# Kernel tuning notes

Hardware: AMD Instinct MI355X
Metric: run time of the kernel (lower is better)

The kernel has to match this reference:

```python
import jax, jax.numpy as jnp
import numpy as np

BS = 2048; N = 16; IN = 128; H = 128; M = 64; A = 32; IMSG = 64; NNH = 256; NA = 30; CB = 64

def _lin(x, w, b):
    return x @ w.T + b

def _bn(x, g, b):
    # BatchNorm1d in training mode: batch statistics, biased variance, eps=1e-5
    m = x.mean(0)
    v = x.var(0)
    return (x - m) / jnp.sqrt(v + 1e-5) * g + b

_lrelu = jax.nn.leaky_relu  # default negative_slope=0.01 matches torch LeakyReLU


def setup_inputs() -> dict:
    key = jax.random.key(0)
    ks = iter(jax.random.split(key, 32))
    def w(shape):
        return jax.random.normal(next(ks), shape, jnp.float32) / np.sqrt(shape[-1]).astype(np.float32)
    R = BS * N
    return {
        'inputs': jax.random.normal(next(ks), (R, IN), jnp.float32),
        'hidden_state': jax.random.normal(next(ks), (R, H), jnp.float32),
        'latent_state': jax.random.normal(next(ks), (R, CB), jnp.float32),
        'eps': jax.random.normal(next(ks), (R, M), jnp.float32),
        'fc1_w': w((H, IN)), 'fc1_b': jnp.zeros((H,), jnp.float32),
        'w_ih': w((3 * H, H)), 'w_hh': w((3 * H, H)),
        'b_ih': jnp.zeros((3 * H,), jnp.float32), 'b_hh': jnp.zeros((3 * H,), jnp.float32),
        'lse_w1': w((H, CB)), 'lse_b1': jnp.zeros((H,), jnp.float32),
        'lse_w2': w((H, H)), 'lse_b2': jnp.zeros((H,), jnp.float32),
        'me_w1': w((NNH, 2 * H)), 'me_b1': jnp.zeros((NNH,), jnp.float32),
        'me_g': jnp.ones((NNH,), jnp.float32), 'me_beta': jnp.zeros((NNH,), jnp.float32),
        'me_w2': w((2 * M, NNH)), 'me_b2': jnp.zeros((2 * M,), jnp.float32),
        'k_w': w((A, H)), 'k_b': jnp.zeros((A,), jnp.float32),
        'q_w': w((A, M)), 'q_b': jnp.zeros((A,), jnp.float32),
        'v_w1': w((NNH, H + M)), 'v_b1': jnp.zeros((NNH,), jnp.float32),
        'v_w2': w((IMSG, NNH)), 'v_b2': jnp.zeros((IMSG,), jnp.float32),
        'fc2_w': w((NA, 2 * H + IMSG * N)), 'fc2_b': jnp.zeros((NA,), jnp.float32),
        'n_agents': N,
    }


def reference(inputs, hidden_state, latent_state, eps,
              fc1_w, fc1_b, w_ih, w_hh, b_ih, b_hh,
              lse_w1, lse_b1, lse_w2, lse_b2,
              me_w1, me_b1, me_g, me_beta, me_w2, me_b2,
              k_w, k_b, q_w, q_b, v_w1, v_b1, v_w2, v_b2,
              fc2_w, fc2_b, n_agents):
    n = n_agents
    R = inputs.shape[0]
    bs = R // n
    # calc_hidden: fc1 + relu, then GRUCell
    x = jax.nn.relu(_lin(inputs, fc1_w, fc1_b))
    gi = _lin(x, w_ih, b_ih)
    gh = _lin(hidden_state, w_hh, b_hh)
    ir, iz, inn = jnp.split(gi, 3, axis=-1)
    hr, hz, hn = jnp.split(gh, 3, axis=-1)
    r = jax.nn.sigmoid(ir + hr)
    z = jax.nn.sigmoid(iz + hz)
    ng = jnp.tanh(inn + r * hn)
    h = ng + z * (hidden_state - ng)  # [R, H]
    # latent_state_encoder
    latent_emb = _lin(jax.nn.relu(_lin(latent_state, lse_w1, lse_b1)), lse_w2, lse_b2)
    le_d = jax.lax.stop_gradient(latent_emb)  # .detach() in source
    # msg_encoder -> clamped Normal params -> rsample
    t = _lrelu(_bn(_lin(jnp.concatenate([h, le_d], -1), me_w1, me_b1), me_g, me_beta))
    t = _lrelu(_lin(t, me_w2, me_b2))
    Md = eps.shape[-1]
    mean = jnp.clip(t[:, :Md], -1.0, 1.0)
    std = jnp.clip(t[:, Md:], 0.5, 1.0)
    pm = mean + std * eps  # personal_msg per agent, [R, M]
    # attn_message_integration: value/query at pair (i,j) depend only on sender j,
    # so compute once per sender and broadcast (same math as repeat in source).
    value = _lin(_lrelu(_lin(jnp.concatenate([h, pm], -1), v_w1, v_b1)), v_w2, v_b2).reshape(bs, n, -1)
    keyv = _lin(h, k_w, k_b).reshape(bs, n, -1)
    qv = _lin(pm, q_w, q_b).reshape(bs, n, -1)
    kh = keyv / jnp.maximum(jnp.linalg.norm(keyv, axis=-1, keepdims=True), 1e-8)
    qh = qv / jnp.maximum(jnp.linalg.norm(qv, axis=-1, keepdims=True), 1e-8)
    alpha = jax.nn.softmax(jnp.einsum('bia,bja->bij', kh, qh), axis=-1)  # cosine attn
    diag_mask = 1.0 - jnp.eye(n, dtype=alpha.dtype)  # zero self-messages
    msg = (alpha * diag_mask)[..., None] * value[:, None, :, :]  # [bs, n, n, IMSG]
    msg = msg.reshape(R, -1)
    return _lin(jnp.concatenate([h, latent_emb, msg], -1), fc2_w, fc2_b)  # q: [R, NA]
```

## Files before the change

### kernel.cpp

```cpp
#include <hip/hip_runtime.h>
#include <math.h>

namespace {
constexpr int R_ = 32768;
constexpr int N_ = 16;
constexpr int NA_ = 30;
constexpr int BSB_ = R_ / N_;
constexpr int NB64_ = R_ / 64;
}

typedef __bf16 bf16x8 __attribute__((ext_vector_type(8)));
typedef float f32x4 __attribute__((ext_vector_type(4)));

__device__ inline unsigned int f2bf(float f) {
    unsigned int u = __float_as_uint(f);
    return (u + 0x7fffu + ((u >> 16) & 1u)) >> 16;
}
__device__ inline float bf2f(unsigned int us) {
    return __uint_as_float(us << 16);
}
__device__ inline unsigned int pack2(float a, float b) {
    return f2bf(a) | (f2bf(b) << 16);
}
__device__ inline uint4 pack8(float4 f0, float4 f1) {
    uint4 u;
    u.x = pack2(f0.x, f0.y); u.y = pack2(f0.z, f0.w);
    u.z = pack2(f1.x, f1.y); u.w = pack2(f1.z, f1.w);
    return u;
}
__device__ inline float fsig(float x)  { return __builtin_amdgcn_rcpf(1.f + __expf(-x)); }
__device__ inline float ftanh(float x) { return 1.f - 2.f * __builtin_amdgcn_rcpf(__expf(2.f * x) + 1.f); }

__device__ __forceinline__ bf16x8 lda_frag(const uint4* At, int KC, int row, int c) {
    return __builtin_bit_cast(bf16x8, At[(row * KC + c) ^ (row & 7)]);
}
__device__ __forceinline__ bf16x8 ldb_frag(const unsigned short* W, int row, int rstride, int c) {
    return __builtin_bit_cast(bf16x8, *(const uint4*)(W + (size_t)row * rstride + (size_t)c * 8));
}

namespace woff {
constexpr unsigned fc1 = 0;
constexpr unsigned ih  = 16384;
constexpr unsigned hh  = 65536;
constexpr unsigned l1  = 114688;
constexpr unsigned l2  = 122880;
constexpr unsigned m1  = 139264;
constexpr unsigned m2  = 204800;
constexpr unsigned kw  = 237568;
constexpr unsigned qw  = 241664;
constexpr unsigned v1  = 243712;
constexpr unsigned v2  = 292864;
constexpr unsigned f2  = 309248;
constexpr unsigned total = 347648;
}

__global__ __launch_bounds__(256)
void wcvt_kernel(const float* __restrict__ fc1_w, const float* __restrict__ w_ih,
                 const float* __restrict__ w_hh, const float* __restrict__ lse_w1,
                 const float* __restrict__ lse_w2, const float* __restrict__ me_w1,
                 const float* __restrict__ me_w2, const float* __restrict__ k_w,
                 const float* __restrict__ q_w, const float* __restrict__ v_w1,
                 const float* __restrict__ v_w2, const float* __restrict__ fc2_w,
                 unsigned short* __restrict__ dst)
{
    unsigned i = blockIdx.x * 256 + threadIdx.x;
    if (i >= woff::total) return;
    const float* src; unsigned base;
    if      (i < woff::ih) { src = fc1_w;  base = woff::fc1; }
    else if (i < woff::hh) { src = w_ih;   base = woff::ih; }
    else if (i < woff::l1) { src = w_hh;   base = woff::hh; }
    else if (i < woff::l2) { src = lse_w1; base = woff::l1; }
    else if (i < woff::m1) { src = lse_w2; base = woff::l2; }
    else if (i < woff::m2) { src = me_w1;  base = woff::m1; }
    else if (i < woff::kw) { src = me_w2;  base = woff::m2; }
    else if (i < woff::qw) { src = k_w;    base = woff::kw; }
    else if (i < woff::v1) { src = q_w;    base = woff::qw; }
    else if (i < woff::v2) { src = v_w1;   base = woff::v1; }
    else if (i < woff::f2) { src = v_w2;   base = woff::v2; }
    else                   { src = fc2_w;  base = woff::f2; }
    dst[i] = (unsigned short)f2bf(src[i - base]);
}

__global__ __launch_bounds__(512, 4)
void stage1(const float* __restrict__ inputs, const float* __restrict__ hidden,
            const unsigned short* __restrict__ fc1w, const float* __restrict__ fc1_b,
            const unsigned short* __restrict__ wih, const unsigned short* __restrict__ whh,
            const float* __restrict__ b_ih, const float* __restrict__ b_hh,
            unsigned short* __restrict__ hb,
            const float* __restrict__ latent,
            const unsigned short* __restrict__ w1b, const float* __restrict__ b1,
            const unsigned short* __restrict__ w2b, const float* __restrict__ b2,
            unsigned short* __restrict__ leb)
{
    __shared__ uint4 shbuf[64 * 48];
    const int tid = threadIdx.x;
    const int lane = tid & 63, w = tid >> 6;
    const int m = lane & 15, g = lane >> 4;

    if (blockIdx.x < (unsigned)NB64_) {
        uint4* Ain   = shbuf;
        uint4* Atile = shbuf + 64 * 16;
        const int r0 = blockIdx.x * 64;

        for (int idx = tid; idx < 64 * 16; idx += 512) {
            int row = idx >> 4, c = idx & 15;
            const float4* p = (const float4*)(inputs + (size_t)(r0 + row) * 128 + c * 8);
            Ain[(row * 16 + c) ^ (row & 7)] = pack8(p[0], p[1]);
            const float4* ph = (const float4*)(hidden + (size_t)(r0 + row) * 128 + c * 8);
            Atile[(row * 32 + (16 + c)) ^ (row & 7)] = pack8(ph[0], ph[1]);
        }
        __syncthreads();

        {
            f32x4 acc[4] = {};
            #pragma unroll
            for (int ks = 0; ks < 4; ++ks) {
                bf16x8 bf = ldb_frag(fc1w, w * 16 + m, 128, ks * 4 + g);
                #pragma unroll
                for (int fr = 0; fr < 4; ++fr) {
                    bf16x8 af = lda_frag(Ain, 16, fr * 16 + m, ks * 4 + g);
                    acc[fr] = __builtin_amdgcn_mfma_f32_16x16x32_bf16(af, bf, acc[fr], 0, 0, 0);
                }
            }
            int col = w * 16 + m;
            float bv = fc1_b[col];
            int c = col >> 3, el = col & 7;
            #pragma unroll
            for (int fr = 0; fr < 4; ++fr) {
                #pragma unroll
                for (int i = 0; i < 4; ++i) {
                    int row = fr * 16 + g * 4 + i;
                    float v = acc[fr][i] + bv;
                    v = v > 0.f ? v : 0.f;
                    ((unsigned short*)Atile)[((row * 32 + c) ^ (row & 7)) * 8 + el] =
                        (unsigned short)f2bf(v);
                }
            }
        }
        __syncthreads();

        {
            f32x4 rr[4] = {}, zz[4] = {}, ni[4] = {}, nh[4] = {};
            const int ro = w * 16 + m;
            #pragma unroll
            for (int ks = 0; ks < 4; ++ks) {
                bf16x8 brr = ldb_frag(wih, ro, 128, ks * 4 + g);
                bf16x8 bzz = ldb_frag(wih, 128 + ro, 128, ks * 4 + g);
                bf16x8 bnn = ldb_frag(wih, 256 + ro, 128, ks * 4 + g);
                #pragma unroll
                for (int fr = 0; fr < 4; ++fr) {
                    bf16x8 af = lda_frag(Atile, 32, fr * 16 + m, ks * 4 + g);
                    rr[fr] = __builtin_amdgcn_mfma_f32_16x16x32_bf16(af, brr, rr[fr], 0, 0, 0);
                    zz[fr] = __builtin_amdgcn_mfma_f32_16x16x32_bf16(af, bzz, zz[fr], 0, 0, 0);
                    ni[fr] = __builtin_amdgcn_mfma_f32_16x16x32_bf16(af, bnn, ni[fr], 0, 0, 0);
                }
            }
            #pragma unroll
            for (int ks = 0; ks < 4; ++ks) {
                bf16x8 brr = ldb_frag(whh, ro, 128, ks * 4 + g);
                bf16x8 bzz = ldb_frag(whh, 128 + ro, 128, ks * 4 + g);
                bf16x8 bnn = ldb_frag(whh, 256 + ro, 128, ks * 4 + g);
                #pragma unroll
                for (int fr = 0; fr < 4; ++fr) {
                    bf16x8 af = lda_frag(Atile, 32, fr * 16 + m, 16 + ks * 4 + g);
                    rr[fr] = __builtin_amdgcn_mfma_f32_16x16x32_bf16(af, brr, rr[fr], 0, 0, 0);
                    zz[fr] = __builtin_amdgcn_mfma_f32_16x16x32_bf16(af, bzz, zz[fr], 0, 0, 0);
                    nh[fr] = __builtin_amdgcn_mfma_f32_16x16x32_bf16(af, bnn, nh[fr], 0, 0, 0);
                }
            }
            {
                int c = ro;
                float brz = b_ih[c] + b_hh[c];
                float bzz2 = b_ih[128 + c] + b_hh[128 + c];
                float bin = b_ih[256 + c], bhn = b_hh[256 + c];
                int hc = 16 + (c >> 3), hel = c & 7;
                #pragma unroll
                for (int fr = 0; fr < 4; ++fr) {
                    #pragma unroll
                    for (int i = 0; i < 4; ++i) {
                        int row = fr * 16 + g * 4 + i;
                        float rv = fsig(rr[fr][i] + brz);
                        float zv = fsig(zz[fr][i] + bzz2);
                        float ng = ftanh(ni[fr][i] + bin + rv * (nh[fr][i] + bhn));
                        float hp = bf2f(((unsigned short*)Atile)[((row * 32 + hc) ^ (row & 7)) * 8 + hel]);
                        float hv = ng + zv * (hp - ng);
                        hb[(size_t)(r0 + row) * 128 + c] = (unsigned short)f2bf(hv);
                    }
                }
            }
        }
    } else {
        uint4* Alat = shbuf;
        uint4* Alt  = shbuf + 64 * 8;
        const int r0 = (blockIdx.x - NB64_) * 64;

        {
            int row = tid >> 3, c = tid & 7;
            const float4* p = (const float4*)(latent + (size_t)(r0 + row) * 64 + c * 8);
            Alat[(row * 8 + c) ^ (row & 7)] = pack8(p[0], p[1]);
        }
        __syncthreads();

        {
            f32x4 acc[4] = {};
            #pragma unroll
            for (int ks = 0; ks < 2; ++ks) {
                bf16x8 bf = ldb_frag(w1b, w * 16 + m, 64, ks * 4 + g);
                #pragma unroll
                for (int fr = 0; fr < 4; ++fr) {
                    bf16x8 af = lda_frag(Alat, 8, fr * 16 + m, ks * 4 + g);
                    acc[fr] = __builtin_amdgcn_mfma_f32_16x16x32_bf16(af, bf, acc[fr], 0, 0, 0);
                }
            }
            int col = w * 16 + m;
            float bv = b1[col];
            int c = col >> 3, el = col & 7;
            #pragma unroll
            for (int fr = 0; fr < 4; ++fr) {
                #pragma unroll
                for (int i = 0; i < 4; ++i) {
                    int row = fr * 16 + g * 4 + i;
                    float v = acc[fr][i] + bv;
                    v = v > 0.f ? v : 0.f;
                    ((unsigned short*)Alt)[((row * 16 + c) ^ (row & 7)) * 8 + el] =
                        (unsigned short)f2bf(v);
                }
            }
        }
        __syncthreads();

        {
            f32x4 acc[4] = {};
            #pragma unroll
            for (int ks = 0; ks < 4; ++ks) {
                bf16x8 bf = ldb_frag(w2b, w * 16 + m, 128, ks * 4 + g);
                #pragma unroll
                for (int fr = 0; fr < 4; ++fr) {
                    bf16x8 af = lda_frag(Alt, 16, fr * 16 + m, ks * 4 + g);
                    acc[fr] = __builtin_amdgcn_mfma_f32_16x16x32_bf16(af, bf, acc[fr], 0, 0, 0);
                }
            }
            int col = w * 16 + m;
            float bv = b2[col];
            #pragma unroll
            for (int fr = 0; fr < 4; ++fr) {
                #pragma unroll
                for (int i = 0; i < 4; ++i) {
                    int rowl = fr * 16 + g * 4 + i;
                    float v = acc[fr][i] + bv;
                    leb[(size_t)(r0 + rowl) * 128 + col] = (unsigned short)f2bf(v);
                }
            }
        }
    }
}

__global__ __launch_bounds__(512, 4)
void me1_stats(const unsigned short* __restrict__ hb, const unsigned short* __restrict__ leb,
               const unsigned short* __restrict__ W, const float* __restrict__ bias,
               const unsigned short* __restrict__ f2w, const float* __restrict__ fc2_b,
               unsigned short* __restrict__ t1,
               float* __restrict__ psum, float* __restrict__ psq,
               float* __restrict__ hl)
{
    __shared__ uint4 Atile[64 * 32];
    __shared__ uint4 T1b[64 * 32];
    const int tid = threadIdx.x;
    const int r0 = blockIdx.x * 64;

    for (int idx = tid; idx < 64 * 16; idx += 512) {
        int row = idx >> 4, c = idx & 15;
        Atile[(row * 32 + c) ^ (row & 7)] =
            *(const uint4*)(hb + (size_t)(r0 + row) * 128 + c * 8);
        Atile[(row * 32 + (16 + c)) ^ (row & 7)] =
            *(const uint4*)(leb + (size_t)(r0 + row) * 128 + c * 8);
    }
    __syncthreads();

    const int lane = tid & 63, w = tid >> 6;
    const int m = lane & 15, g = lane >> 4;
    unsigned short* t1s = (unsigned short*)T1b;

    {
        const int o0 = w * 32;
        f32x4 acc[4][2] = {};
        #pragma unroll
        for (int ks = 0; ks < 8; ++ks) {
            bf16x8 bf[2];
            #pragma unroll
            for (int fc = 0; fc < 2; ++fc)
                bf[fc] = ldb_frag(W, o0 + fc * 16 + m, 256, ks * 4 + g);
            #pragma unroll
            for (int fr = 0; fr < 4; ++fr) {
                bf16x8 af = lda_frag(Atile, 32, fr * 16 + m, ks * 4 + g);
                #pragma unroll
                for (int fc = 0; fc < 2; ++fc)
                    acc[fr][fc] = __builtin_amdgcn_mfma_f32_16x16x32_bf16(
                        af, bf[fc], acc[fr][fc], 0, 0, 0);
            }
        }
        #pragma unroll
        for (int fc = 0; fc < 2; ++fc) {
            int col = o0 + fc * 16 + m;
            float bv = bias[col];
            float s = 0.f, q = 0.f;
            #pragma unroll
            for (int fr = 0; fr < 4; ++fr) {
                #pragma unroll
                for (int i = 0; i < 4; ++i) {
                    int rowl = fr * 16 + g * 4 + i;
                    float v = acc[fr][fc][i] + bv;
                    t1s[rowl * 256 + col] = (unsigned short)f2bf(v);
                    s += v; q += v * v;
                }
            }
            s += __shfl_xor(s, 16); s += __shfl_xor(s, 32);
            q += __shfl_xor(q, 16); q += __shfl_xor(q, 32);
            if (lane < 16) {
                psum[(size_t)blockIdx.x * 256 + col] = s;
                psq[(size_t)blockIdx.x * 256 + col] = q;
            }
        }
    }
    __syncthreads();
    for (int idx = tid; idx < 64 * 32; idx += 512) {
        int row = idx >> 5, c = idx & 31;
        *(uint4*)(t1 + (size_t)(r0 + row) * 256 + c * 8) = T1b[row * 32 + c];
    }

    if (w < 4) {
        f32x4 acc[2] = {};
        #pragma unroll
        for (int ks = 0; ks < 8; ++ks) {
            bf16x8 af = lda_frag(Atile, 32, w * 16 + m, ks * 4 + g);
            bf16x8 bf[2];
            #pragma unroll
            for (int fc = 0; fc < 2; ++fc) {
                int col = fc * 16 + m;
                bf[fc] = (col < NA_) ? ldb_frag(f2w, col, 1280, ks * 4 + g) : bf16x8{};
            }
            #pragma unroll
            for (int fc = 0; fc < 2; ++fc)
                acc[fc] = __builtin_amdgcn_mfma_f32_16x16x32_bf16(af, bf[fc], acc[fc], 0, 0, 0);
        }
        #pragma unroll
        for (int fc = 0; fc < 2; ++fc) {
            int col = fc * 16 + m;
            if (col < NA_) {
                float bv = fc2_b[col];
                #pragma unroll
                for (int i = 0; i < 4; ++i) {
                    int row = r0 + w * 16 + g * 4 + i;
                    hl[(size_t)row * NA_ + col] = acc[fc][i] + bv;
                }
            }
        }
    }
}

__global__ __launch_bounds__(256)
void bn_final_kernel(const float* __restrict__ psum, const float* __restrict__ psq,
                     const float* __restrict__ g, const float* __restrict__ beta,
                     float* __restrict__ scale, float* __restrict__ shift)
{
    __shared__ float redS[4], redQ[4];
    const int f = blockIdx.x;
    const int tid = threadIdx.x;
    float s = 0.f, q = 0.f;
    for (int b = tid; b < NB64_; b += 256) {
        s += psum[(size_t)b * 256 + f];
        q += psq[(size_t)b * 256 + f];
    }
    #pragma unroll
    for (int off = 32; off >= 1; off >>= 1) {
        s += __shfl_down(s, off);
        q += __shfl_down(q, off);
    }
    if ((tid & 63) == 0) { redS[tid >> 6] = s; redQ[tid >> 6] = q; }
    __syncthreads();
    if (tid == 0) {
        s = redS[0] + redS[1] + redS[2] + redS[3];
        q = redQ[0] + redQ[1] + redQ[2] + redQ[3];
        float mean = s / (float)R_;
        float var = q / (float)R_ - mean * mean;
        float istd = rsqrtf(var + 1e-5f);
        float sc = g[f] * istd;
        scale[f] = sc;
        shift[f] = beta[f] - mean * sc;
    }
}

__global__ __launch_bounds__(512, 4)
void me2kqv(const unsigned short* __restrict__ t1,
            const float* __restrict__ scale, const float* __restrict__ shift,
            const unsigned short* __restrict__ W2, const float* __restrict__ me2_b,
            const float* __restrict__ eps,
            const unsigned short* __restrict__ hb,
            const unsigned short* __restrict__ kwb, const float* __restrict__ k_b,
            const unsigned short* __restrict__ qwb, const float* __restrict__ q_b,
            const unsigned short* __restrict__ v1w, const float* __restrict__ v1_b,
            const unsigned short* __restrict__ v2w, const float* __restrict__ v2_b,
            unsigned short* __restrict__ kh, unsigned short* __restrict__ qh,
            unsigned short* __restrict__ valb)
{
    __shared__ uint4 bufA[64 * 32];
    __shared__ uint4 bufB[64 * 24];
    __shared__ float sc_s[256], sh_s[256];
    const int tid = threadIdx.x;
    const int r0 = blockIdx.x * 64;
    const int lane = tid & 63, w = tid >> 6;
    const int m = lane & 15, g = lane >> 4;

    if (tid < 256) { sc_s[tid] = scale[tid]; sh_s[tid] = shift[tid]; }
    for (int idx = tid; idx < 64 * 16; idx += 512) {
        int row = idx >> 4, c = idx & 15;
        bufB[(row * 24 + c) ^ (row & 7)] =
            *(const uint4*)(hb + (size_t)(r0 + row) * 128 + c * 8);
    }
    __syncthreads();

    for (int idx = tid; idx < 64 * 32; idx += 512) {
        int row = idx >> 5, c = idx & 31;
        uint4 u = *(const uint4*)(t1 + (size_t)(r0 + row) * 256 + c * 8);
        unsigned int vv[4] = {u.x, u.y, u.z, u.w};
        float f[8];
        #pragma unroll
        for (int q2 = 0; q2 < 4; ++q2) {
            f[2 * q2]     = __uint_as_float((vv[q2] & 0xffffu) << 16);
            f[2 * q2 + 1] = __uint_as_float(vv[q2] & 0xffff0000u);
        }
        int k = c * 8;
        #pragma unroll
        for (int j = 0; j < 8; ++j) {
            float v = f[j] * sc_s[k + j] + sh_s[k + j];
            f[j] = v > 0.f ? v : 0.01f * v;
        }
        uint4 r;
        r.x = pack2(f[0], f[1]); r.y = pack2(f[2], f[3]);
        r.z = pack2(f[4], f[5]); r.w = pack2(f[6], f[7]);
        bufA[(row * 32 + c) ^ (row & 7)] = r;
    }
    __syncthreads();

    {
        const int colm = w * 16 + m;
        f32x4 acc[4] = {};
        #pragma unroll
        for (int ks = 0; ks < 8; ++ks) {
            bf16x8 bf = ldb_frag(W2, colm, 256, ks * 4 + g);
            #pragma unroll
            for (int fr = 0; fr < 4; ++fr) {
                bf16x8 af = lda_frag(bufA, 32, fr * 16 + m, ks * 4 + g);
                acc[fr] = __builtin_amdgcn_mfma_f32_16x16x32_bf16(af, bf, acc[fr], 0, 0, 0);
            }
        }
        float bv = me2_b[colm];
        __syncthreads();
        float* meanS = (float*)bufA;
        if (w < 4) {
            #pragma unroll
            for (int fr = 0; fr < 4; ++fr) {
                #pragma unroll
                for (int i = 0; i < 4; ++i) {
                    int row = fr * 16 + g * 4 + i;
                    float vm = acc[fr][i] + bv;
                    vm = vm > 0.f ? vm : 0.01f * vm;
                    vm = fminf(fmaxf(vm, -1.f), 1.f);
                    meanS[row * 64 + colm] = vm;
                }
            }
        }
        __syncthreads();
        if (w >= 4) {
            int cp = colm - 64;
            int hc = 16 + (cp >> 3), hel = cp & 7;
            #pragma unroll
            for (int fr = 0; fr < 4; ++fr) {
                #pragma unroll
                for (int i = 0; i < 4; ++i) {
                    int row = fr * 16 + g * 4 + i;
                    float vs = acc[fr][i] + bv;
                    vs = vs > 0.f ? vs : 0.01f * vs;
                    vs = fminf(fmaxf(vs, 0.5f), 1.f);
                    float e = eps[(size_t)(r0 + row) * 64 + cp];
                    float vm = meanS[row * 64 + cp];
                    ((unsigned short*)bufB)[((row * 24 + hc) ^ (row & 7)) * 8 + hel] =
                        (unsigned short)f2bf(vm + vs * e);
                }
            }
        }
    }
    __syncthreads();

    if (w < 4) {
        const bool isq = (w >= 2);
        const int rbase = (w & 1) * 32;
        f32x4 acc[2][2] = {};
        const int nks = isq ? 2 : 4;
        for (int ks = 0; ks < nks; ++ks) {
            bf16x8 af[2], bf[2];
            #pragma unroll
            for (int fr = 0; fr < 2; ++fr)
                af[fr] = lda_frag(bufB, 24, rbase + fr * 16 + m, (isq ? 16 : 0) + ks * 4 + g);
            #pragma unroll
            for (int fc = 0; fc < 2; ++fc)
                bf[fc] = isq ? ldb_frag(qwb, fc * 16 + m, 64, ks * 4 + g)
                             : ldb_frag(kwb, fc * 16 + m, 128, ks * 4 + g);
            #pragma unroll
            for (int fr = 0; fr < 2; ++fr)
                #pragma unroll
                for (int fc = 0; fc < 2; ++fc)
                    acc[fr][fc] = __builtin_amdgcn_mfma_f32_16x16x32_bf16(
                        af[fr], bf[fc], acc[fr][fc], 0, 0, 0);
        }
        const float* bias = isq ? q_b : k_b;
        float b0 = bias[m], b1 = bias[16 + m];
        unsigned short* outp = isq ? qh : kh;
        #pragma unroll
        for (int fr = 0; fr < 2; ++fr) {
            #pragma unroll
            for (int i = 0; i < 4; ++i) {
                float v0 = acc[fr][0][i] + b0;
                float v1 = acc[fr][1][i] + b1;
                float ss = v0 * v0 + v1 * v1;
                ss += __shfl_xor(ss, 1); ss += __shfl_xor(ss, 2);
                ss += __shfl_xor(ss, 4); ss += __shfl_xor(ss, 8);
                float inv = 1.f / fmaxf(sqrtf(ss), 1e-8f);
                int row = r0 + rbase + fr * 16 + g * 4 + i;
                outp[(size_t)row * 32 + m] = (unsigned short)f2bf(v0 * inv);
                outp[(size_t)row * 32 + 16 + m] = (unsigned short)f2bf(v1 * inv);
            }
        }
    }

    {
        const int o0 = w * 32;
        f32x4 acc[4][2] = {};
        #pragma unroll
        for (int ks = 0; ks < 6; ++ks) {
            bf16x8 bf[2];
            #pragma unroll
            for (int fc = 0; fc < 2; ++fc)
                bf[fc] = ldb_frag(v1w, o0 + fc * 16 + m, 192, ks * 4 + g);
            #pragma unroll
            for (int fr = 0; fr < 4; ++fr) {
                bf16x8 af = lda_frag(bufB, 24, fr * 16 + m, ks * 4 + g);
                #pragma unroll
                for (int fc = 0; fc < 2; ++fc)
                    acc[fr][fc] = __builtin_amdgcn_mfma_f32_16x16x32_bf16(
                        af, bf[fc], acc[fr][fc], 0, 0, 0);
            }
        }
        #pragma unroll
        for (int fc = 0; fc < 2; ++fc) {
            int col = o0 + fc * 16 + m;
            float bv = v1_b[col];
            int c = col >> 3, el = col & 7;
            #pragma unroll
            for (int fr = 0; fr < 4; ++fr) {
                #pragma unroll
                for (int i = 0; i < 4; ++i) {
                    int row = fr * 16 + g * 4 + i;
                    float v = acc[fr][fc][i] + bv;
                    v = v > 0.f ? v : 0.01f * v;
                    ((unsigned short*)bufA)[((row * 32 + c) ^ (row & 7)) * 8 + el] =
                        (unsigned short)f2bf(v);
                }
            }
        }
    }
    __syncthreads();

    {
        const int col = (w & 3) * 16 + m;
        const int rbase = (w >> 2) * 32;
        f32x4 acc[2] = {};
        #pragma unroll
        for (int ks = 0; ks < 8; ++ks) {
            bf16x8 bf = ldb_frag(v2w, col, 256, ks * 4 + g);
            #pragma unroll
            for (int fr = 0; fr < 2; ++fr) {
                bf16x8 af = lda_frag(bufA, 32, rbase + fr * 16 + m, ks * 4 + g);
                acc[fr] = __builtin_amdgcn_mfma_f32_16x16x32_bf16(af, bf, acc[fr], 0, 0, 0);
            }
        }
        float bv = v2_b[col];
        unsigned short* vb = (unsigned short*)bufB;
        #pragma unroll
        for (int fr = 0; fr < 2; ++fr) {
            #pragma unroll
            for (int i = 0; i < 4; ++i) {
                int rowl = rbase + fr * 16 + g * 4 + i;
                vb[rowl * 64 + col] = (unsigned short)f2bf(acc[fr][i] + bv);
            }
        }
    }
    __syncthreads();
    {
        int row = tid >> 3, c = tid & 7;
        *(uint4*)(valb + (size_t)(r0 + row) * 64 + c * 8) = ((uint4*)bufB)[row * 8 + c];
    }
}

__global__ __launch_bounds__(256)
void vproj_kernel(const unsigned short* __restrict__ value, const float* __restrict__ w2,
                  float* __restrict__ vproj)
{
    __shared__ float w2s[NA_][65];
    __shared__ float val_s[64][65];
    const int tid = threadIdx.x;
    const int j = blockIdx.x & 15;
    const int b0 = (blockIdx.x >> 4) * 64;

    for (int idx = tid; idx < NA_ * 64; idx += 256) {
        int na = idx >> 6, k = idx & 63;
        w2s[na][k] = w2[(size_t)na * 1280 + 256 + j * 64 + k];
    }
    for (int idx = tid; idx < 64 * 64; idx += 256) {
        int bl = idx >> 6, k = idx & 63;
        val_s[bl][k] = bf2f(value[((size_t)(b0 + bl) * 16 + j) * 64 + k]);
    }
    __syncthreads();

    for (int task = tid; task < 64 * NA_; task += 256) {
        int bl = task / NA_, na = task - bl * NA_;
        float acc = 0.f;
        #pragma unroll 16
        for (int k = 0; k < 64; ++k) acc = fmaf(val_s[bl][k], w2s[na][k], acc);
        vproj[((size_t)(b0 + bl) * 16 + j) * NA_ + na] = acc;
    }
}

__global__ __launch_bounds__(256)
void attn_combine(const unsigned short* __restrict__ kh, const unsigned short* __restrict__ qh,
                  const float* __restrict__ vproj, const float* __restrict__ hl,
                  float* __restrict__ outv)
{
    __shared__ float kh_s[16][33], qh_s[16][33];
    __shared__ float al_s[16][16];
    __shared__ float vp_s[16][NA_];
    const int tid = threadIdx.x;
    const size_t rb = (size_t)blockIdx.x * 16;

    for (int idx = tid; idx < 512; idx += 256) {
        int r = idx >> 5, a = idx & 31;
        kh_s[r][a] = bf2f(kh[rb * 32 + idx]);
        qh_s[r][a] = bf2f(qh[rb * 32 + idx]);
    }
    for (int idx = tid; idx < 16 * NA_; idx += 256)
        vp_s[idx / NA_][idx % NA_] = vproj[rb * NA_ + idx];
    __syncthreads();

    {
        int i = tid >> 4, j = tid & 15;
        float l = 0.f;
        #pragma unroll
        for (int a = 0; a < 32; ++a) l = fmaf(kh_s[i][a], qh_s[j][a], l);
        float mx = l;
        #pragma unroll
        for (int mm = 8; mm >= 1; mm >>= 1) mx = fmaxf(mx, __shfl_xor(mx, mm));
        float e = __expf(l - mx);
        float s = e;
        #pragma unroll
        for (int mm = 8; mm >= 1; mm >>= 1) s += __shfl_xor(s, mm);
        float a = e / s;
        if (i == j) a = 0.f;
        al_s[i][j] = a;
    }
    __syncthreads();

    for (int task = tid; task < 16 * NA_; task += 256) {
        int i = task / NA_, na = task - i * NA_;
        float acc = hl[(rb + i) * NA_ + na];
        #pragma unroll
        for (int j = 0; j < 16; ++j) acc = fmaf(al_s[i][j], vp_s[j][na], acc);
        outv[(rb + i) * NA_ + na] = acc;
    }
}

extern "C" void kernel_launch(void* const* d_in, const int* in_sizes, int n_in,
                              void* d_out, int out_size, void* d_ws, size_t ws_size,
                              hipStream_t stream)
{
    (void)in_sizes; (void)n_in; (void)out_size; (void)ws_size;
    const float* inputs  = (const float*)d_in[0];
    const float* hidden  = (const float*)d_in[1];
    const float* latent  = (const float*)d_in[2];
    const float* eps     = (const float*)d_in[3];
    const float* fc1_w   = (const float*)d_in[4];
    const float* fc1_b   = (const float*)d_in[5];
    const float* w_ih    = (const float*)d_in[6];
    const float* w_hh    = (const float*)d_in[7];
    const float* b_ih    = (const float*)d_in[8];
    const float* b_hh    = (const float*)d_in[9];
    const float* lse_w1  = (const float*)d_in[10];
    const float* lse_b1  = (const float*)d_in[11];
    const float* lse_w2  = (const float*)d_in[12];
    const float* lse_b2  = (const float*)d_in[13];
    const float* me_w1   = (const float*)d_in[14];
    const float* me_b1   = (const float*)d_in[15];
    const float* me_g    = (const float*)d_in[16];
    const float* me_beta = (const float*)d_in[17];
    const float* me_w2   = (const float*)d_in[18];
    const float* me_b2   = (const float*)d_in[19];
    const float* k_w     = (const float*)d_in[20];
    const float* k_b     = (const float*)d_in[21];
    const float* q_w     = (const float*)d_in[22];
    const float* q_b     = (const float*)d_in[23];
    const float* v_w1    = (const float*)d_in[24];
    const float* v_b1    = (const float*)d_in[25];
    const float* v_w2    = (const float*)d_in[26];
    const float* v_b2    = (const float*)d_in[27];
    const float* fc2_w   = (const float*)d_in[28];
    const float* fc2_b   = (const float*)d_in[29];

    const size_t R = R_;
    unsigned short* bws = (unsigned short*)d_ws;
    unsigned short* hb   = bws;
    unsigned short* leb  = hb + R * 128;
    unsigned short* t1b  = leb + R * 128;
    unsigned short* valb = t1b + R * 256;
    unsigned short* khb  = valb + R * 64;
    unsigned short* qhb  = khb + R * 32;
    unsigned short* wb   = qhb + R * 32;
    float* fws  = (float*)(wb + woff::total);
    float* hlf  = fws;
    float* vpf  = hlf + R * 30;
    float* psum = vpf + R * 30;
    float* psq  = psum + (size_t)NB64_ * 256;
    float* scale = psq + (size_t)NB64_ * 256;
    float* shift = scale + 256;

    dim3 blk(256);
    dim3 g512(NB64_);

    wcvt_kernel<<<dim3((woff::total + 255) / 256), blk, 0, stream>>>(
        fc1_w, w_ih, w_hh, lse_w1, lse_w2, me_w1, me_w2, k_w, q_w, v_w1, v_w2, fc2_w, wb);

    stage1<<<dim3(2 * NB64_), dim3(512), 0, stream>>>(
        inputs, hidden, wb + woff::fc1, fc1_b, wb + woff::ih, wb + woff::hh,
        b_ih, b_hh, hb,
        latent, wb + woff::l1, lse_b1, wb + woff::l2, lse_b2, leb);
    me1_stats<<<g512, dim3(512), 0, stream>>>(hb, leb, wb + woff::m1, me_b1,
                                              wb + woff::f2, fc2_b, t1b, psum, psq, hlf);
    bn_final_kernel<<<dim3(256), blk, 0, stream>>>(psum, psq, me_g, me_beta, scale, shift);
    me2kqv<<<g512, dim3(512), 0, stream>>>(t1b, scale, shift, wb + woff::m2, me_b2, eps,
                                           hb, wb + woff::kw, k_b, wb + woff::qw, q_b,
                                           wb + woff::v1, v_b1, wb + woff::v2, v_b2,
                                           khb, qhb, valb);
    vproj_kernel<<<dim3(16 * (BSB_ / 64)), blk, 0, stream>>>(valb, fc2_w, vpf);
    attn_combine<<<dim3(BSB_), blk, 0, stream>>>(khb, qhb, vpf, hlf, (float*)d_out);
}
```

Baseline: 108.9 us.

## Fuse value projection and attention combine into one MFMA tail kernel

Replaces the separate vproj and attn_combine kernels with a single attn_tail kernel handling 8 batches per block. The cosine attention logits and the value-by-fc2 projection now run on bf16 MFMA instructions, and the fp32 vproj intermediate is kept in shared memory instead of being written to and read back from global memory. This removes one launch and a global round trip. In exchange the projection uses bf16 fc2 weights, and the 16-row MFMA tiles waste half their rows on 8 batches.

```diff
diff --git a/kernel.cpp b/kernel.cpp
--- a/kernel.cpp
+++ b/kernel.cpp
@@ -602,79 +602,86 @@
     }
 }
 
-__global__ __launch_bounds__(256)
-void vproj_kernel(const unsigned short* __restrict__ value, const float* __restrict__ w2,
-                  float* __restrict__ vproj)
+__global__ __launch_bounds__(512, 4)
+void attn_tail(const unsigned short* __restrict__ khb, const unsigned short* __restrict__ qhb,
+               const unsigned short* __restrict__ valb,
+               const unsigned short* __restrict__ f2wb,
+               const float* __restrict__ hl, float* __restrict__ outv)
 {
-    __shared__ float w2s[NA_][65];
-    __shared__ float val_s[64][65];
+    __shared__ uint4 vt[136 * 8];
+    __shared__ float al[128 * 16];
+    __shared__ float vp[128 * 32];
     const int tid = threadIdx.x;
-    const int j = blockIdx.x & 15;
-    const int b0 = (blockIdx.x >> 4) * 64;
-
-    for (int idx = tid; idx < NA_ * 64; idx += 256) {
-        int na = idx >> 6, k = idx & 63;
-        w2s[na][k] = w2[(size_t)na * 1280 + 256 + j * 64 + k];
-    }
-    for (int idx = tid; idx < 64 * 64; idx += 256) {
-        int bl = idx >> 6, k = idx & 63;
-        val_s[bl][k] = bf2f(value[((size_t)(b0 + bl) * 16 + j) * 64 + k]);
-    }
-    __syncthreads();
-
-    for (int task = tid; task < 64 * NA_; task += 256) {
-        int bl = task / NA_, na = task - bl * NA_;
-        float acc = 0.f;
-        #pragma unroll 16
-        for (int k = 0; k < 64; ++k) acc = fmaf(val_s[bl][k], w2s[na][k], acc);
-        vproj[((size_t)(b0 + bl) * 16 + j) * NA_ + na] = acc;
-    }
-}
-
-__global__ __launch_bounds__(256)
-void attn_combine(const unsigned short* __restrict__ kh, const unsigned short* __restrict__ qh,
-                  const float* __restrict__ vproj, const float* __restrict__ hl,
-                  float* __restrict__ outv)
-{
-    __shared__ float kh_s[16][33], qh_s[16][33];
-    __shared__ float al_s[16][16];
-    __shared__ float vp_s[16][NA_];
-    const int tid = threadIdx.x;
-    const size_t rb = (size_t)blockIdx.x * 16;
-
-    for (int idx = tid; idx < 512; idx += 256) {
-        int r = idx >> 5, a = idx & 31;
-        kh_s[r][a] = bf2f(kh[rb * 32 + idx]);
-        qh_s[r][a] = bf2f(qh[rb * 32 + idx]);
-    }
-    for (int idx = tid; idx < 16 * NA_; idx += 256)
-        vp_s[idx / NA_][idx % NA_] = vproj[rb * NA_ + idx];
-    __syncthreads();
+    const int b0 = blockIdx.x * 8;
+    const size_t r0 = (size_t)b0 * 16;
+    const int lane = tid & 63, w = tid >> 6;
+    const int m = lane & 15, g = lane >> 4;
+
+    for (int idx = tid; idx < 128 * 8; idx += 512) {
+        int r = idx >> 3, c = idx & 7;
+        int bi = r >> 4, j = r & 15;
+        int vr = j * 8 + bi;
+        vt[(vr * 8 + c) ^ (vr & 7)] = *(const uint4*)(valb + (r0 + r) * 64 + c * 8);
+    }
 
     {
-        int i = tid >> 4, j = tid & 15;
-        float l = 0.f;
-        #pragma unroll
-        for (int a = 0; a < 32; ++a) l = fmaf(kh_s[i][a], qh_s[j][a], l);
-        float mx = l;
-        #pragma unroll
-        for (int mm = 8; mm >= 1; mm >>= 1) mx = fmaxf(mx, __shfl_xor(mx, mm));
-        float e = __expf(l - mx);
-        float s = e;
-        #pragma unroll
-        for (int mm = 8; mm >= 1; mm >>= 1) s += __shfl_xor(s, mm);
-        float a = e / s;
-        if (i == j) a = 0.f;
-        al_s[i][j] = a;
-    }
-    __syncthreads();
-
-    for (int task = tid; task < 16 * NA_; task += 256) {
-        int i = task / NA_, na = task - i * NA_;
-        float acc = hl[(rb + i) * NA_ + na];
-        #pragma unroll
-        for (int j = 0; j < 16; ++j) acc = fmaf(al_s[i][j], vp_s[j][na], acc);
-        outv[(rb + i) * NA_ + na] = acc;
+        bf16x8 af = ldb_frag(khb, (b0 + w) * 16 + m, 32, g);
+        bf16x8 bf = ldb_frag(qhb, (b0 + w) * 16 + m, 32, g);
+        f32x4 acc = {};
+        acc = __builtin_amdgcn_mfma_f32_16x16x32_bf16(af, bf, acc, 0, 0, 0);
+        #pragma unroll
+        for (int i = 0; i < 4; ++i) {
+            float l = acc[i];
+            float mx = l;
+            #pragma unroll
+            for (int mm = 8; mm >= 1; mm >>= 1) mx = fmaxf(mx, __shfl_xor(mx, mm));
+            float e = __expf(l - mx);
+            float s = e;
+            #pragma unroll
+            for (int mm = 8; mm >= 1; mm >>= 1) s += __shfl_xor(s, mm);
+            float a = e / s;
+            int ip = g * 4 + i;
+            if (ip == m) a = 0.f;
+            al[(w * 16 + ip) * 16 + m] = a;
+        }
+    }
+    __syncthreads();
+
+    #pragma unroll
+    for (int jj = 0; jj < 2; ++jj) {
+        int j = w + jj * 8;
+        f32x4 acc[2] = {};
+        #pragma unroll
+        for (int ks = 0; ks < 2; ++ks) {
+            bf16x8 af = lda_frag(vt, 8, j * 8 + (m & 7), ks * 4 + g);
+            #pragma unroll
+            for (int fc = 0; fc < 2; ++fc) {
+                bf16x8 bf = ldb_frag(f2wb, fc * 16 + m, 1280, 32 + j * 8 + ks * 4 + g);
+                acc[fc] = __builtin_amdgcn_mfma_f32_16x16x32_bf16(af, bf, acc[fc], 0, 0, 0);
+            }
+        }
+        #pragma unroll
+        for (int fc = 0; fc < 2; ++fc) {
+            int na = fc * 16 + m;
+            if (na < NA_) {
+                #pragma unroll
+                for (int i = 0; i < 4; ++i) {
+                    int bi = g * 4 + i;
+                    if (bi < 8) vp[(j * 8 + bi) * 32 + na] = acc[fc][i];
+                }
+            }
+        }
+    }
+    __syncthreads();
+
+    for (int task = tid; task < 128 * NA_; task += 512) {
+        int row = task / NA_, na = task - row * NA_;
+        int bi = row >> 4;
+        float acc = hl[(r0 + row) * NA_ + na];
+        #pragma unroll
+        for (int j = 0; j < 16; ++j)
+            acc = fmaf(al[row * 16 + j], vp[(j * 8 + bi) * 32 + na], acc);
+        outv[(r0 + row) * NA_ + na] = acc;
     }
 }
 
@@ -725,8 +732,7 @@
     unsigned short* wb   = qhb + R * 32;
     float* fws  = (float*)(wb + woff::total);
     float* hlf  = fws;
-    float* vpf  = hlf + R * 30;
-    float* psum = vpf + R * 30;
+    float* psum = hlf + R * 30;
     float* psq  = psum + (size_t)NB64_ * 256;
     float* scale = psq + (size_t)NB64_ * 256;
     float* shift = scale + 256;
@@ -748,6 +754,6 @@
                                            hb, wb + woff::kw, k_b, wb + woff::qw, q_b,
                                            wb + woff::v1, v_b1, wb + woff::v2, v_b2,
                                            khb, qhb, valb);
-    vproj_kernel<<<dim3(16 * (BSB_ / 64)), blk, 0, stream>>>(valb, fc2_w, vpf);
-    attn_combine<<<dim3(BSB_), blk, 0, stream>>>(khb, qhb, vpf, hlf, (float*)d_out);
-}
+    attn_tail<<<dim3(BSB_ / 8), dim3(512), 0, stream>>>(
+        khb, qhb, valb, wb + woff::f2, hlf, (float*)d_out);
+}
```

New measurement: 94.37 us (median of 2 runs). 13.3% less time.
